# Kernel optimization log

Hardware: AMD Instinct MI355X
Metric: run time of the kernel (lower is better)

## Reference

```python
import jax, jax.numpy as jnp
import numpy as np

B, C, W, H = 4, 256, 64, 64
DK = C // 8  # query/key channels


def setup_inputs() -> dict:
    key = jax.random.key(0)
    ks = jax.random.split(key, 7)
    x = jax.random.normal(ks[0], (B, C, W, H), dtype=jnp.float32)
    # conv1x1 weights stored as [out_ch, in_ch]
    Wq = jax.random.normal(ks[1], (DK, C), dtype=jnp.float32) / np.sqrt(C)
    bq = jnp.zeros((DK,), dtype=jnp.float32)
    Wk = jax.random.normal(ks[2], (DK, C), dtype=jnp.float32) / np.sqrt(C)
    bk = jnp.zeros((DK,), dtype=jnp.float32)
    Wv = jax.random.normal(ks[3], (C, C), dtype=jnp.float32) / np.sqrt(C)
    bv = jnp.zeros((C,), dtype=jnp.float32)
    gamma = jnp.zeros((1,), dtype=jnp.float32)
    return {"x": x, "Wq": Wq, "bq": bq, "Wk": Wk, "bk": bk,
            "Wv": Wv, "bv": bv, "gamma": gamma}


def reference(x, Wq, bq, Wk, bk, Wv, bv, gamma):
    b, c, w, h = x.shape
    n = w * h
    xf = x.reshape(b, c, n)                     # [B, C, N]
    # conv1x1 == channel matmul
    q = jnp.einsum('dc,bcn->bnd', Wq, xf) + bq  # [B, N, DK]
    k = jnp.einsum('dc,bcn->bdn', Wk, xf) + bk[None, :, None]  # [B, DK, N]
    energy = jnp.einsum('bnd,bdm->bnm', q, k)   # [B, N, N]
    attention = jax.nn.softmax(energy, axis=-1)
    v = jnp.einsum('dc,bcn->bdn', Wv, xf) + bv[None, :, None]  # [B, C, N]
    out = jnp.einsum('bdm,bnm->bdn', v, attention)              # [B, C, N]
    out = out.reshape(b, c, w, h)
    out = gamma * out + x
    return out, attention
```

## Files before the change

### kernel.cpp

```cpp
#include <hip/hip_runtime.h>
#include <hip/hip_bf16.h>

typedef __attribute__((ext_vector_type(8))) short bf16x8;
typedef __attribute__((ext_vector_type(4))) float f32x4;
typedef __attribute__((ext_vector_type(4))) unsigned int u32x4;
typedef __attribute__((ext_vector_type(2))) unsigned int u32x2;

#define B_SZ 4
#define C_SZ 256
#define N_SZ 4096
#define DK_SZ 32

#define WQB_OFF 0
#define WKB_OFF 8192
#define WVB_OFF 16384
#define QB_OFF  81920
#define KB_OFF  606208
#define VB_OFF  1130496

__device__ __forceinline__ short f2bf(float f) {
    union { float f; unsigned int u; } v; v.f = f;
    unsigned int r = v.u + 0x7fffu + ((v.u >> 16) & 1u);
    return (short)(r >> 16);
}

__device__ __forceinline__ unsigned int cvt_pk_bf16(float lo, float hi) {
    unsigned int r;
    asm volatile("v_cvt_pk_bf16_f32 %0, %1, %2" : "=v"(r) : "v"(lo), "v"(hi));
    return r;
}

__device__ __forceinline__ f32x4 mfma16(bf16x8 a, bf16x8 b, f32x4 c) {
    return __builtin_amdgcn_mfma_f32_16x16x32_bf16(a, b, c, 0, 0, 0);
}

__device__ __forceinline__ void gload_lds16(const void* g, void* l) {
    __builtin_amdgcn_global_load_lds((const __attribute__((address_space(1))) unsigned int*)g,
                                     (__attribute__((address_space(3))) unsigned int*)l, 16, 0, 0);
}

__device__ __forceinline__ void remap_block(int i, int& b, int& n0) {
    b = (i & 7) >> 1;
    n0 = (((i >> 3) << 1) | (i & 1)) * 64;
}

__global__ __launch_bounds__(256) void k_convw(const float* __restrict__ Wq,
                                               const float* __restrict__ Wk,
                                               const float* __restrict__ Wv,
                                               short* __restrict__ ws) {
    int i = blockIdx.x * 256 + threadIdx.x;
    if (i < 8192) {
        ws[WQB_OFF + i] = f2bf(Wq[i]);
        ws[WKB_OFF + i] = f2bf(Wk[i]);
    }
    ws[WVB_OFF + i] = f2bf(Wv[i]);
}

__global__ __launch_bounds__(256) void k_prep(const float* __restrict__ x,
                                              const float* __restrict__ bq,
                                              const float* __restrict__ bk,
                                              const float* __restrict__ bv,
                                              short* __restrict__ ws) {
    __shared__ short xsT[64][264];
    __shared__ short vt_s[64][258];

    int b, n0;
    remap_block(blockIdx.x, b, n0);
    const int t = threadIdx.x;
    const float* xb = x + (size_t)b * C_SZ * N_SZ;

    {
        int c0 = t >> 4, n4 = (t & 15) * 4;
#pragma unroll
        for (int i = 0; i < 16; i++) {
            int c = c0 + 16 * i;
            float4 v = *(const float4*)(xb + (size_t)c * N_SZ + n0 + n4);
            xsT[n4 + 0][c] = f2bf(v.x);
            xsT[n4 + 1][c] = f2bf(v.y);
            xsT[n4 + 2][c] = f2bf(v.z);
            xsT[n4 + 3][c] = f2bf(v.w);
        }
    }
    __syncthreads();

    const int w = t >> 6, l = t & 63;
    const int lr = l & 15, lk = l >> 4;

    bf16x8 af[8];
#pragma unroll
    for (int kk = 0; kk < 8; kk++)
        af[kk] = *(const bf16x8*)(&xsT[w * 16 + lr][kk * 32 + lk * 8]);

#pragma unroll
    for (int qk = 0; qk < 2; qk++) {
        const short* wb = ws + (qk ? WKB_OFF : WQB_OFF);
        const float* bias = qk ? bk : bq;
        short* outp = ws + (qk ? KB_OFF : QB_OFF) + (size_t)b * N_SZ * DK_SZ;
#pragma unroll
        for (int cf = 0; cf < 2; cf++) {
            f32x4 acc = {0.f, 0.f, 0.f, 0.f};
#pragma unroll
            for (int kk = 0; kk < 8; kk++) {
                bf16x8 bfr = *(const bf16x8*)(wb + (cf * 16 + lr) * 256 + kk * 32 + lk * 8);
                acc = mfma16(af[kk], bfr, acc);
            }
            float bias_v = bias[cf * 16 + lr];
#pragma unroll
            for (int r = 0; r < 4; r++) {
                int row = w * 16 + lk * 4 + r;
                outp[(size_t)(n0 + row) * DK_SZ + cf * 16 + lr] = f2bf(acc[r] + bias_v);
            }
        }
    }

#pragma unroll
    for (int cf = 0; cf < 16; cf++) {
        f32x4 acc = {0.f, 0.f, 0.f, 0.f};
#pragma unroll
        for (int kk = 0; kk < 8; kk++) {
            bf16x8 bfr = *(const bf16x8*)(ws + WVB_OFF + (cf * 16 + lr) * 256 + kk * 32 + lk * 8);
            acc = mfma16(af[kk], bfr, acc);
        }
        float bias_v = bv[cf * 16 + lr];
#pragma unroll
        for (int r = 0; r < 4; r++) {
            vt_s[w * 16 + lk * 4 + r][cf * 16 + lr] = f2bf(acc[r] + bias_v);
        }
    }
    __syncthreads();
    {
        short* vb = ws + VB_OFF + (size_t)b * C_SZ * N_SZ;
        int nn = t & 63;
#pragma unroll
        for (int i = 0; i < 64; i++) {
            int c = (t >> 6) + 4 * i;
            vb[(size_t)c * N_SZ + n0 + nn] = vt_s[nn][c];
        }
    }
}

__global__ __launch_bounds__(512, 1) void k_attn(const short* __restrict__ ws,
                                                 const float* __restrict__ x,
                                                 const float* __restrict__ gamma_p,
                                                 float* __restrict__ out) {
    __shared__ short v_lds[3][16384];
    __shared__ short k_lds[3][2304];
    __shared__ short p_lds[2][64][72];
    __shared__ float rsum_s[2][64];

    int b, n0;
    remap_block(blockIdx.x, b, n0);
    const int t = threadIdx.x, w = t >> 6, l = t & 63;
    const int rg = w & 3, ch = w >> 2;
    const int rp = w & 1, cp = w >> 1;
    const int lr = l & 15, lk = l >> 4;

    const short* qb = ws + QB_OFF + (size_t)b * N_SZ * DK_SZ;
    const short* kb = ws + KB_OFF + (size_t)b * N_SZ * DK_SZ;
    const short* vb = ws + VB_OFF + (size_t)b * C_SZ * N_SZ;
    const char* kbb = (const char*)kb;

    bf16x8 qf = *(const bf16x8*)(qb + (size_t)(n0 + rg * 16 + lr) * DK_SZ + lk * 8);

    float rs = 0.f;
    for (int mt = 0; mt < 32; mt++) {
        int mb = ch * 2048 + mt * 64;
        bf16x8 kfa = *(const bf16x8*)(kb + (size_t)(mb + lr) * DK_SZ + lk * 8);
        bf16x8 kfb = *(const bf16x8*)(kb + (size_t)(mb + 16 + lr) * DK_SZ + lk * 8);
        bf16x8 kfc = *(const bf16x8*)(kb + (size_t)(mb + 32 + lr) * DK_SZ + lk * 8);
        bf16x8 kfd = *(const bf16x8*)(kb + (size_t)(mb + 48 + lr) * DK_SZ + lk * 8);
        f32x4 s0 = mfma16(kfa, qf, (f32x4){0.f, 0.f, 0.f, 0.f});
        f32x4 s1 = mfma16(kfb, qf, (f32x4){0.f, 0.f, 0.f, 0.f});
        f32x4 s2 = mfma16(kfc, qf, (f32x4){0.f, 0.f, 0.f, 0.f});
        f32x4 s3 = mfma16(kfd, qf, (f32x4){0.f, 0.f, 0.f, 0.f});
#pragma unroll
        for (int r = 0; r < 4; r++)
            rs += __expf(s0[r]) + __expf(s1[r]) + __expf(s2[r]) + __expf(s3[r]);
    }
    rs += __shfl_xor(rs, 16);
    rs += __shfl_xor(rs, 32);
    if (l < 16) rsum_s[ch][rg * 16 + l] = rs;
    __syncthreads();
    const float invp = 1.f / (rsum_s[0][rg * 16 + lr] + rsum_s[1][rg * 16 + lr]);

    float* attn_row = out + (size_t)B_SZ * C_SZ * N_SZ + (size_t)b * N_SZ * N_SZ
                      + (size_t)(n0 + rg * 16 + lr) * N_SZ;
    f32x4 O[2][4];
#pragma unroll
    for (int rf = 0; rf < 2; rf++)
#pragma unroll
        for (int cb = 0; cb < 4; cb++) O[rf][cb] = (f32x4){0.f, 0.f, 0.f, 0.f};

    f32x4 e0, e1;
    int sc_mbase = 0;

#define STAGE(tt, buf)                                                             \
    {                                                                              \
        gload_lds16(kbb + (size_t)(tt) * 4096 + w * 512 + l * 16,                  \
                    (void*)&k_lds[buf][w * 256]);                                  \
        const int mb = (tt) * 64;                                                  \
        _Pragma("unroll")                                                          \
        for (int i = 0; i < 4; i++) {                                              \
            int c = w * 32 + i * 8 + (l >> 3);                                     \
            int j = l & 7;                                                         \
            const short* g = vb + (size_t)c * N_SZ + mb + ((j ^ (c & 7)) << 3);    \
            gload_lds16(g, (void*)&v_lds[buf][(w * 32 + i * 8) * 64]);             \
        }                                                                          \
    }

#define SCOMP_CALC(tt, pb)                                                         \
    {                                                                              \
        sc_mbase = (tt) * 64 + ch * 32;                                            \
        const char* kl = (const char*)&k_lds[(tt) % 3][0];                         \
        bf16x8 kf0 = *(const bf16x8*)(kl + (ch * 32 + lr) * 64 + lk * 16);         \
        bf16x8 kf1 = *(const bf16x8*)(kl + (ch * 32 + 16 + lr) * 64 + lk * 16);    \
        f32x4 s0 = mfma16(kf0, qf, (f32x4){0.f, 0.f, 0.f, 0.f});                   \
        f32x4 s1 = mfma16(kf1, qf, (f32x4){0.f, 0.f, 0.f, 0.f});                   \
        e0[0] = __expf(s0[0]) * invp; e0[1] = __expf(s0[1]) * invp;                \
        e0[2] = __expf(s0[2]) * invp; e0[3] = __expf(s0[3]) * invp;                \
        e1[0] = __expf(s1[0]) * invp; e1[1] = __expf(s1[1]) * invp;                \
        e1[2] = __expf(s1[2]) * invp; e1[3] = __expf(s1[3]) * invp;                \
        u32x2 pk0, pk1;                                                            \
        pk0[0] = cvt_pk_bf16(e0[0], e0[1]); pk0[1] = cvt_pk_bf16(e0[2], e0[3]);    \
        pk1[0] = cvt_pk_bf16(e1[0], e1[1]); pk1[1] = cvt_pk_bf16(e1[2], e1[3]);    \
        *(u32x2*)(&p_lds[pb][rg * 16 + lr][ch * 32 + lk * 4]) = pk0;               \
        *(u32x2*)(&p_lds[pb][rg * 16 + lr][ch * 32 + 16 + lk * 4]) = pk1;          \
    }

#define SSTORE()                                                                   \
    {                                                                              \
        __builtin_nontemporal_store(e0, (f32x4*)(attn_row + sc_mbase + lk * 4));   \
        __builtin_nontemporal_store(e1, (f32x4*)(attn_row + sc_mbase + 16 + lk * 4)); \
    }

    STAGE(0, 0);
    STAGE(1, 1);
    __builtin_amdgcn_sched_barrier(0);
    asm volatile("s_waitcnt vmcnt(9)" ::: "memory");
    __builtin_amdgcn_sched_barrier(0);
    SCOMP_CALC(0, 0);
    SSTORE();

    for (int mt = 0; mt < 64; mt++) {
        asm volatile("s_waitcnt vmcnt(2) lgkmcnt(0)" ::: "memory");
        __builtin_amdgcn_sched_barrier(0);
        __builtin_amdgcn_s_barrier();
        __builtin_amdgcn_sched_barrier(0);
        const int cur = mt & 1;
        if (mt < 63) SCOMP_CALC(mt + 1, cur ^ 1);
        __builtin_amdgcn_sched_barrier(0);
        if (mt < 62) STAGE(mt + 2, (mt + 2) % 3);
        __builtin_amdgcn_sched_barrier(0);
        if (mt < 63) SSTORE();
        __builtin_amdgcn_sched_barrier(0);
        const int vcur = mt % 3;
        const char* pbase = (const char*)&p_lds[cur][rp * 32 + lr][0];
        bf16x8 a00 = *(const bf16x8*)(pbase + lk * 16);
        bf16x8 a01 = *(const bf16x8*)(pbase + 64 + lk * 16);
        bf16x8 a10 = *(const bf16x8*)(pbase + 2304 + lk * 16);
        bf16x8 a11 = *(const bf16x8*)(pbase + 2304 + 64 + lk * 16);
        const char* vbase = (const char*)&v_lds[vcur][0];
#pragma unroll
        for (int cb = 0; cb < 4; cb++) {
            int c = cp * 64 + cb * 16 + lr;
            int sw = (c & 7) << 4;
            bf16x8 b0 = *(const bf16x8*)(vbase + c * 128 + ((lk << 4) ^ sw));
            bf16x8 b1 = *(const bf16x8*)(vbase + c * 128 + (((4 + lk) << 4) ^ sw));
            O[0][cb] = mfma16(a00, b0, O[0][cb]);
            O[0][cb] = mfma16(a01, b1, O[0][cb]);
            O[1][cb] = mfma16(a10, b0, O[1][cb]);
            O[1][cb] = mfma16(a11, b1, O[1][cb]);
        }
    }
#undef STAGE
#undef SCOMP_CALC
#undef SSTORE

    __syncthreads();
    const float g = gamma_p[0];
    float* o_s = (float*)&v_lds[0][0];
    const float* xb = x + (size_t)b * C_SZ * N_SZ;
    float* ob = out + (size_t)b * C_SZ * N_SZ;
#pragma unroll
    for (int half = 0; half < 2; half++) {
        if (rp == half) {
#pragma unroll
            for (int rf = 0; rf < 2; rf++)
#pragma unroll
                for (int cb = 0; cb < 4; cb++)
#pragma unroll
                    for (int r = 0; r < 4; r++)
                        o_s[(rf * 16 + lk * 4 + r) * 258 + cp * 64 + cb * 16 + lr] = O[rf][cb][r];
        }
        __syncthreads();
        {
            int nn = t & 31;
            int c0 = t >> 5;
#pragma unroll
            for (int i = 0; i < 16; i++) {
                int c = c0 + 16 * i;
                size_t idx = (size_t)c * N_SZ + n0 + half * 32 + nn;
                ob[idx] = g * o_s[nn * 258 + c] + xb[idx];
            }
        }
        __syncthreads();
    }
}

extern "C" void kernel_launch(void* const* d_in, const int* in_sizes, int n_in,
                              void* d_out, int out_size, void* d_ws, size_t ws_size,
                              hipStream_t stream) {
    const float* x     = (const float*)d_in[0];
    const float* Wq    = (const float*)d_in[1];
    const float* bq    = (const float*)d_in[2];
    const float* Wk    = (const float*)d_in[3];
    const float* bk    = (const float*)d_in[4];
    const float* Wv    = (const float*)d_in[5];
    const float* bv    = (const float*)d_in[6];
    const float* gamma = (const float*)d_in[7];
    short* ws = (short*)d_ws;
    float* out = (float*)d_out;

    hipLaunchKernelGGL(k_convw, dim3(256), dim3(256), 0, stream, Wq, Wk, Wv, ws);
    hipLaunchKernelGGL(k_prep, dim3(256), dim3(256), 0, stream, x, bq, bk, bv, ws);
    hipLaunchKernelGGL(k_attn, dim3(256), dim3(512), 0, stream, ws, x, gamma, out);
}
```

Baseline: 147.1 us.

## Keep softmax probabilities in registers via lane shuffles and split PV across key halves

```diff
diff --git a/kernel.cpp b/kernel.cpp
--- a/kernel.cpp
+++ b/kernel.cpp
@@ -145,14 +145,12 @@
                                                  float* __restrict__ out) {
     __shared__ short v_lds[3][16384];
     __shared__ short k_lds[3][2304];
-    __shared__ short p_lds[2][64][72];
     __shared__ float rsum_s[2][64];
 
     int b, n0;
     remap_block(blockIdx.x, b, n0);
     const int t = threadIdx.x, w = t >> 6, l = t & 63;
     const int rg = w & 3, ch = w >> 2;
-    const int rp = w & 1, cp = w >> 1;
     const int lr = l & 15, lk = l >> 4;
 
     const short* qb = ws + QB_OFF + (size_t)b * N_SZ * DK_SZ;
@@ -185,125 +183,147 @@
 
     float* attn_row = out + (size_t)B_SZ * C_SZ * N_SZ + (size_t)b * N_SZ * N_SZ
                       + (size_t)(n0 + rg * 16 + lr) * N_SZ;
-    f32x4 O[2][4];
-#pragma unroll
-    for (int rf = 0; rf < 2; rf++)
-#pragma unroll
-        for (int cb = 0; cb < 4; cb++) O[rf][cb] = (f32x4){0.f, 0.f, 0.f, 0.f};
-
-    f32x4 e0, e1;
-    int sc_mbase = 0;
-
-#define STAGE(tt, buf)                                                             \
-    {                                                                              \
-        gload_lds16(kbb + (size_t)(tt) * 4096 + w * 512 + l * 16,                  \
-                    (void*)&k_lds[buf][w * 256]);                                  \
-        const int mb = (tt) * 64;                                                  \
-        _Pragma("unroll")                                                          \
-        for (int i = 0; i < 4; i++) {                                              \
-            int c = w * 32 + i * 8 + (l >> 3);                                     \
-            int j = l & 7;                                                         \
-            const short* g = vb + (size_t)c * N_SZ + mb + ((j ^ (c & 7)) << 3);    \
-            gload_lds16(g, (void*)&v_lds[buf][(w * 32 + i * 8) * 64]);             \
-        }                                                                          \
-    }
-
-#define SCOMP_CALC(tt, pb)                                                         \
-    {                                                                              \
-        sc_mbase = (tt) * 64 + ch * 32;                                            \
-        const char* kl = (const char*)&k_lds[(tt) % 3][0];                         \
-        bf16x8 kf0 = *(const bf16x8*)(kl + (ch * 32 + lr) * 64 + lk * 16);         \
-        bf16x8 kf1 = *(const bf16x8*)(kl + (ch * 32 + 16 + lr) * 64 + lk * 16);    \
-        f32x4 s0 = mfma16(kf0, qf, (f32x4){0.f, 0.f, 0.f, 0.f});                   \
-        f32x4 s1 = mfma16(kf1, qf, (f32x4){0.f, 0.f, 0.f, 0.f});                   \
-        e0[0] = __expf(s0[0]) * invp; e0[1] = __expf(s0[1]) * invp;                \
-        e0[2] = __expf(s0[2]) * invp; e0[3] = __expf(s0[3]) * invp;                \
-        e1[0] = __expf(s1[0]) * invp; e1[1] = __expf(s1[1]) * invp;                \
-        e1[2] = __expf(s1[2]) * invp; e1[3] = __expf(s1[3]) * invp;                \
-        u32x2 pk0, pk1;                                                            \
-        pk0[0] = cvt_pk_bf16(e0[0], e0[1]); pk0[1] = cvt_pk_bf16(e0[2], e0[3]);    \
-        pk1[0] = cvt_pk_bf16(e1[0], e1[1]); pk1[1] = cvt_pk_bf16(e1[2], e1[3]);    \
-        *(u32x2*)(&p_lds[pb][rg * 16 + lr][ch * 32 + lk * 4]) = pk0;               \
-        *(u32x2*)(&p_lds[pb][rg * 16 + lr][ch * 32 + 16 + lk * 4]) = pk1;          \
-    }
-
-#define SSTORE()                                                                   \
-    {                                                                              \
-        __builtin_nontemporal_store(e0, (f32x4*)(attn_row + sc_mbase + lk * 4));   \
-        __builtin_nontemporal_store(e1, (f32x4*)(attn_row + sc_mbase + 16 + lk * 4)); \
+    f32x4 O[16];
+#pragma unroll
+    for (int cb = 0; cb < 16; cb++) O[cb] = (f32x4){0.f, 0.f, 0.f, 0.f};
+
+    const bool odd = lk & 1;
+    const bool swp = ((lk >> 1) ^ (lk & 1)) & 1;
+    const bool hi  = lk >> 1;
+    const int krow = ch * 32 + lr;
+    const int kswz = ((lk ^ ((lr >> 1) & 3)) << 4);
+    const int voff = lr * 128 + ((((ch << 2) + lk) ^ (lr & 7)) << 4);
+
+    bf16x8 kf0, kf1, pf, pfN;
+
+#define STAGE(tt, buf)                                                              \
+    {                                                                               \
+        const int krw = w * 8 + (l >> 2);                                           \
+        const int ksl = (l & 3) ^ ((l >> 3) & 3);                                   \
+        gload_lds16(kbb + (size_t)(tt) * 4096 + krw * 64 + ksl * 16,                \
+                    (void*)&k_lds[buf][w * 256]);                                   \
+        const int mb = (tt) * 64;                                                   \
+        _Pragma("unroll")                                                           \
+        for (int i = 0; i < 4; i++) {                                               \
+            int c = w * 32 + i * 8 + (l >> 3);                                      \
+            int j = l & 7;                                                          \
+            const short* gp = vb + (size_t)c * N_SZ + mb + ((j ^ (c & 7)) << 3);    \
+            gload_lds16(gp, (void*)&v_lds[buf][(w * 32 + i * 8) * 64]);             \
+        }                                                                           \
+    }
+
+#define KREAD(tt)                                                                   \
+    {                                                                               \
+        const char* kl = (const char*)&k_lds[(tt) % 3][0];                          \
+        kf0 = *(const bf16x8*)(kl + krow * 64 + kswz);                              \
+        kf1 = *(const bf16x8*)(kl + krow * 64 + 1024 + kswz);                       \
+    }
+
+#define SCOMP_BODY(tt)                                                              \
+    {                                                                               \
+        f32x4 s0 = mfma16(kf0, qf, (f32x4){0.f, 0.f, 0.f, 0.f});                    \
+        f32x4 s1 = mfma16(kf1, qf, (f32x4){0.f, 0.f, 0.f, 0.f});                    \
+        f32x4 ev0, ev1;                                                             \
+        ev0[0] = __expf(s0[0]) * invp; ev0[1] = __expf(s0[1]) * invp;               \
+        ev0[2] = __expf(s0[2]) * invp; ev0[3] = __expf(s0[3]) * invp;               \
+        ev1[0] = __expf(s1[0]) * invp; ev1[1] = __expf(s1[1]) * invp;               \
+        ev1[2] = __expf(s1[2]) * invp; ev1[3] = __expf(s1[3]) * invp;               \
+        const int mbase = (tt) * 64 + ch * 32 + 4 * lk;                             \
+        __builtin_nontemporal_store(ev0, (f32x4*)(attn_row + mbase));               \
+        __builtin_nontemporal_store(ev1, (f32x4*)(attn_row + mbase + 16));          \
+        unsigned pkA0 = cvt_pk_bf16(ev0[0], ev0[1]);                                \
+        unsigned pkA1 = cvt_pk_bf16(ev0[2], ev0[3]);                                \
+        unsigned pkB0 = cvt_pk_bf16(ev1[0], ev1[1]);                                \
+        unsigned pkB1 = cvt_pk_bf16(ev1[2], ev1[3]);                                \
+        unsigned sw0 = odd ? pkA0 : pkB0;                                           \
+        unsigned sw1 = odd ? pkA1 : pkB1;                                           \
+        unsigned R0 = __shfl_xor(sw0, 16);                                          \
+        unsigned R1 = __shfl_xor(sw1, 16);                                          \
+        unsigned Kp0 = odd ? pkB0 : pkA0;                                           \
+        unsigned Kp1 = odd ? pkB1 : pkA1;                                           \
+        unsigned x0 = __shfl_xor(Kp0, 48); Kp0 = swp ? x0 : Kp0;                    \
+        unsigned x1 = __shfl_xor(Kp1, 48); Kp1 = swp ? x1 : Kp1;                    \
+        unsigned x2 = __shfl_xor(R0, 48);  R0  = swp ? x2 : R0;                     \
+        unsigned x3 = __shfl_xor(R1, 48);  R1  = swp ? x3 : R1;                     \
+        u32x4 pw;                                                                   \
+        pw[0] = hi ? R0 : Kp0; pw[1] = hi ? R1 : Kp1;                               \
+        pw[2] = hi ? Kp0 : R0; pw[3] = hi ? Kp1 : R1;                               \
+        pfN = __builtin_bit_cast(bf16x8, pw);                                       \
     }
 
     STAGE(0, 0);
     STAGE(1, 1);
     __builtin_amdgcn_sched_barrier(0);
-    asm volatile("s_waitcnt vmcnt(9)" ::: "memory");
+    asm volatile("s_waitcnt vmcnt(5)" ::: "memory");
     __builtin_amdgcn_sched_barrier(0);
-    SCOMP_CALC(0, 0);
-    SSTORE();
+    __builtin_amdgcn_s_barrier();
+    KREAD(0);
+    SCOMP_BODY(0);
+    pf = pfN;
 
     for (int mt = 0; mt < 64; mt++) {
         asm volatile("s_waitcnt vmcnt(2) lgkmcnt(0)" ::: "memory");
         __builtin_amdgcn_sched_barrier(0);
         __builtin_amdgcn_s_barrier();
         __builtin_amdgcn_sched_barrier(0);
-        const int cur = mt & 1;
-        if (mt < 63) SCOMP_CALC(mt + 1, cur ^ 1);
-        __builtin_amdgcn_sched_barrier(0);
+        const char* vbase = (const char*)&v_lds[mt % 3][0];
+        if (mt < 63) KREAD(mt + 1);
+        bf16x8 A1[8];
+#pragma unroll
+        for (int cb = 0; cb < 8; cb++)
+            A1[cb] = *(const bf16x8*)(vbase + cb * 2048 + voff);
         if (mt < 62) STAGE(mt + 2, (mt + 2) % 3);
         __builtin_amdgcn_sched_barrier(0);
-        if (mt < 63) SSTORE();
+        if (mt < 63) SCOMP_BODY(mt + 1);
         __builtin_amdgcn_sched_barrier(0);
-        const int vcur = mt % 3;
-        const char* pbase = (const char*)&p_lds[cur][rp * 32 + lr][0];
-        bf16x8 a00 = *(const bf16x8*)(pbase + lk * 16);
-        bf16x8 a01 = *(const bf16x8*)(pbase + 64 + lk * 16);
-        bf16x8 a10 = *(const bf16x8*)(pbase + 2304 + lk * 16);
-        bf16x8 a11 = *(const bf16x8*)(pbase + 2304 + 64 + lk * 16);
-        const char* vbase = (const char*)&v_lds[vcur][0];
-#pragma unroll
-        for (int cb = 0; cb < 4; cb++) {
-            int c = cp * 64 + cb * 16 + lr;
-            int sw = (c & 7) << 4;
-            bf16x8 b0 = *(const bf16x8*)(vbase + c * 128 + ((lk << 4) ^ sw));
-            bf16x8 b1 = *(const bf16x8*)(vbase + c * 128 + (((4 + lk) << 4) ^ sw));
-            O[0][cb] = mfma16(a00, b0, O[0][cb]);
-            O[0][cb] = mfma16(a01, b1, O[0][cb]);
-            O[1][cb] = mfma16(a10, b0, O[1][cb]);
-            O[1][cb] = mfma16(a11, b1, O[1][cb]);
-        }
+        bf16x8 A2[8];
+#pragma unroll
+        for (int cb = 0; cb < 8; cb++)
+            A2[cb] = *(const bf16x8*)(vbase + (cb + 8) * 2048 + voff);
+#pragma unroll
+        for (int cb = 0; cb < 8; cb++) O[cb] = mfma16(A1[cb], pf, O[cb]);
+#pragma unroll
+        for (int cb = 0; cb < 8; cb++) O[cb + 8] = mfma16(A2[cb], pf, O[cb + 8]);
+        pf = pfN;
     }
 #undef STAGE
-#undef SCOMP_CALC
-#undef SSTORE
-
-    __syncthreads();
-    const float g = gamma_p[0];
-    float* o_s = (float*)&v_lds[0][0];
-    const float* xb = x + (size_t)b * C_SZ * N_SZ;
-    float* ob = out + (size_t)b * C_SZ * N_SZ;
-#pragma unroll
-    for (int half = 0; half < 2; half++) {
-        if (rp == half) {
-#pragma unroll
-            for (int rf = 0; rf < 2; rf++)
-#pragma unroll
-                for (int cb = 0; cb < 4; cb++)
-#pragma unroll
-                    for (int r = 0; r < 4; r++)
-                        o_s[(rf * 16 + lk * 4 + r) * 258 + cp * 64 + cb * 16 + lr] = O[rf][cb][r];
-        }
-        __syncthreads();
-        {
-            int nn = t & 31;
-            int c0 = t >> 5;
-#pragma unroll
-            for (int i = 0; i < 16; i++) {
-                int c = c0 + 16 * i;
-                size_t idx = (size_t)c * N_SZ + n0 + half * 32 + nn;
-                ob[idx] = g * o_s[nn * 258 + c] + xb[idx];
+#undef KREAD
+#undef SCOMP_BODY
+
+    __syncthreads();
+    float* o_red = (float*)&v_lds[0][0];
+    const int RSTRIDE = 4360;
+    if (ch == 1) {
+#pragma unroll
+        for (int cb = 0; cb < 16; cb++)
+#pragma unroll
+            for (int r = 0; r < 4; r++)
+                o_red[rg * RSTRIDE + (cb * 16 + 4 * lk + r) * 17 + lr] = O[cb][r];
+    }
+    __syncthreads();
+    if (ch == 0) {
+#pragma unroll
+        for (int cb = 0; cb < 16; cb++)
+#pragma unroll
+            for (int r = 0; r < 4; r++) {
+                int idx = rg * RSTRIDE + (cb * 16 + 4 * lk + r) * 17 + lr;
+                o_red[idx] += O[cb][r];
             }
-        }
-        __syncthreads();
+    }
+    __syncthreads();
+    {
+        const float g = gamma_p[0];
+        const float* xb = x + (size_t)b * C_SZ * N_SZ;
+        float* ob = out + (size_t)b * C_SZ * N_SZ;
+        int nn = t & 63;
+        int c0 = t >> 6;
+        int rbase = (nn >> 4) * RSTRIDE + (nn & 15);
+#pragma unroll
+        for (int i = 0; i < 32; i++) {
+            int c = c0 + 8 * i;
+            size_t idx = (size_t)c * N_SZ + n0 + nn;
+            ob[idx] = g * o_red[rbase + c * 17] + xb[idx];
+        }
     }
 }
 
```

New measurement: 137.4 us. -6.6%, faster.
